# Performance work log

Measured on AMD Instinct MI355X. Metric: run time of the kernel, lower is better.

The kernel has to match this reference:

```python
import jax, jax.numpy as jnp
import numpy as np

D_MODEL, HEADS, D_FF = 1024, 16, 4096
D_K = D_MODEL // HEADS
EPS = 1e-5


def layer_norm(x, g, b):
    mu = jnp.mean(x, axis=-1, keepdims=True)
    var = jnp.mean((x - mu) ** 2, axis=-1, keepdims=True)
    return (x - mu) * jax.lax.rsqrt(var + EPS) * g + b


def setup_inputs() -> dict:
    key = jax.random.key(0)
    ks = jax.random.split(key, 16)
    B, S = 2, 2048
    s = 0.02
    return {
        "src": jax.random.normal(ks[0], (B, S, D_MODEL), jnp.float32),
        "corr": jax.random.normal(ks[1], (B, S, S), jnp.float32),
        "pos": jax.random.normal(ks[2], (B, S, D_MODEL), jnp.float32),
        "Wq": jax.random.normal(ks[3], (D_MODEL, D_MODEL), jnp.float32) * s,
        "bq": jnp.zeros((D_MODEL,), jnp.float32),
        "Wk": jax.random.normal(ks[4], (D_MODEL, D_MODEL), jnp.float32) * s,
        "bk": jnp.zeros((D_MODEL,), jnp.float32),
        "Wv": jax.random.normal(ks[5], (D_MODEL, D_MODEL), jnp.float32) * s,
        "bv": jnp.zeros((D_MODEL,), jnp.float32),
        "Wo": jax.random.normal(ks[6], (D_MODEL, D_MODEL), jnp.float32) * s,
        "bo": jnp.zeros((D_MODEL,), jnp.float32),
        "W1": jax.random.normal(ks[7], (D_MODEL, D_FF), jnp.float32) * s,
        "b1": jnp.zeros((D_FF,), jnp.float32),
        "W2": jax.random.normal(ks[8], (D_FF, D_MODEL), jnp.float32) * s,
        "b2": jnp.zeros((D_MODEL,), jnp.float32),
        "g1": jnp.ones((D_MODEL,), jnp.float32),
        "be1": jnp.zeros((D_MODEL,), jnp.float32),
        "g2": jnp.ones((D_MODEL,), jnp.float32),
        "be2": jnp.zeros((D_MODEL,), jnp.float32),
    }


def reference(src, corr, pos, Wq, bq, Wk, bk, Wv, bv, Wo, bo, W1, b1, W2, b2, g1, be1, g2, be2):
    B, S, _ = src.shape
    qk_in = src + pos  # with_pos_embed for q and k; value uses raw src
    # QKV projections -> [B, H, S, d_k]
    def split_heads(x):
        return x.reshape(B, S, HEADS, D_K).transpose(0, 2, 1, 3)
    q = split_heads(qk_in @ Wq + bq)
    k = split_heads(qk_in @ Wk + bk)
    v = split_heads(src @ Wv + bv)
    # scores [B, H, S, S] with additive correlation bias before softmax
    scores = jnp.einsum("bhqd,bhkd->bhqk", q, k) / jnp.sqrt(jnp.float32(D_K))
    scores = scores + corr[:, None, :, :]
    attn = jax.nn.softmax(scores, axis=-1)
    ctx = jnp.einsum("bhqk,bhkd->bhqd", attn, v)
    concat = ctx.transpose(0, 2, 1, 3).reshape(B, S, D_MODEL)
    attn_out = concat @ Wo + bo
    # post-norm residual blocks (dropout = identity in eval)
    x = layer_norm(src + attn_out, g1, be1)
    ffn = jax.nn.relu(x @ W1 + b1) @ W2 + b2
    x = layer_norm(x + ffn, g2, be2)
    return x
```

## Files before the change

### kernel.cpp

```cpp
#include <hip/hip_runtime.h>
#include <hip/hip_bf16.h>

#define S_LEN  2048
#define BATCH  2
#define DMODEL 1024
#define NHEAD  16
#define DHEAD  64
#define DFF    4096
#define NTOK   (BATCH * S_LEN)
#define QKVLD  3072

typedef __attribute__((ext_vector_type(8))) short short8;
typedef __attribute__((ext_vector_type(4))) short short4v;
typedef __attribute__((ext_vector_type(4))) float f32x4;

__device__ __forceinline__ short f2bs(float f) {
  __hip_bfloat16 h = __float2bfloat16(f);
  short s;
  __builtin_memcpy(&s, &h, sizeof(short));
  return s;
}

__device__ __forceinline__ f32x4 mfma16(short8 a, short8 b, f32x4 c) {
  return __builtin_amdgcn_mfma_f32_16x16x32_bf16(a, b, c, 0, 0, 0);
}

__device__ __forceinline__ void load_lds16(const short* g, short* l) {
  __builtin_amdgcn_global_load_lds(
      (const __attribute__((address_space(1))) void*)g,
      (__attribute__((address_space(3))) void*)l, 16, 0, 0);
}

__global__ void transpose_cast(const float* __restrict__ in, short* __restrict__ out,
                               int R, int C, float scale) {
  __shared__ float tile[32][33];
  const int c0 = blockIdx.x * 32, r0 = blockIdx.y * 32;
  const int tx = threadIdx.x, ty = threadIdx.y;
#pragma unroll
  for (int i = 0; i < 32; i += 8)
    tile[ty + i][tx] = in[(size_t)(r0 + ty + i) * C + c0 + tx];
  __syncthreads();
#pragma unroll
  for (int i = 0; i < 32; i += 8)
    out[(size_t)(c0 + ty + i) * R + r0 + tx] = f2bs(tile[tx][ty + i] * scale);
}

__global__ __launch_bounds__(256) void transpose_bf16(
    const short* __restrict__ in, short* __restrict__ out, int R, int LDin) {
  __shared__ __attribute__((aligned(16))) short tile[64][72];
  const int c0 = blockIdx.x * 64, r0 = blockIdx.y * 64;
#pragma unroll
  for (int i = 0; i < 2; i++) {
    const int idx = threadIdx.x + 256 * i;
    const int rr = idx >> 3, cc8 = (idx & 7) * 8;
    *(int4*)(&tile[rr][cc8]) = *(const int4*)(in + (size_t)(r0 + rr) * LDin + c0 + cc8);
  }
  __syncthreads();
#pragma unroll
  for (int i = 0; i < 2; i++) {
    const int idx = threadIdx.x + 256 * i;
    const int rr = idx >> 3, cc8 = (idx & 7) * 8;
    short8 v;
#pragma unroll
    for (int j = 0; j < 8; j++) v[j] = tile[cc8 + j][rr];
    *(short8*)(out + (size_t)(c0 + rr) * R + r0 + cc8) = v;
  }
}

__global__ void concat_bias(const float* __restrict__ bq, const float* __restrict__ bk,
                            const float* __restrict__ bv, float* __restrict__ bqkv) {
  const int i = blockIdx.x * 256 + threadIdx.x;
  float v;
  if (i < DMODEL) v = bq[i] * 0.125f;
  else if (i < 2 * DMODEL) v = bk[i - DMODEL];
  else v = bv[i - 2 * DMODEL];
  bqkv[i] = v;
}

__global__ void prep_tokens(const float* __restrict__ src, const float* __restrict__ pos,
                            short* __restrict__ qkb, short* __restrict__ srcb) {
  const int i = (blockIdx.x * blockDim.x + threadIdx.x) * 4;
  float4 s = *(const float4*)(src + i);
  float4 p = *(const float4*)(pos + i);
  short4v q4 = {f2bs(s.x + p.x), f2bs(s.y + p.y), f2bs(s.z + p.z), f2bs(s.w + p.w)};
  short4v s4 = {f2bs(s.x), f2bs(s.y), f2bs(s.z), f2bs(s.w)};
  *(short4v*)(qkb + i) = q4;
  *(short4v*)(srcb + i) = s4;
}

template <int RELU, int OUT_BF16>
__global__ __launch_bounds__(256) void gemm_bt(
    const short* __restrict__ A0, const short* __restrict__ A1,
    const short* __restrict__ Bt, const float* __restrict__ bias,
    float* __restrict__ Cf, short* __restrict__ Cb,
    int M, int N, int K, int splitcol) {
  __shared__ __attribute__((aligned(16))) short As[128 * 32];
  __shared__ __attribute__((aligned(16))) short Bs[128 * 32];

  const int tid = threadIdx.x;
  const int wave = tid >> 6, lane = tid & 63;
  const int lm = lane & 15, lq = lane >> 4;
  const int row0 = blockIdx.y * 128, col0 = blockIdx.x * 128;
  const int wr = (wave >> 1) * 64, wc = (wave & 1) * 64;

  const short* A = (col0 < splitcol) ? A0 : A1;
  const short* ag = A + (size_t)(row0 + wave * 32 + (lane >> 2)) * K + (lane & 3) * 8;
  const short* bg = Bt + (size_t)(col0 + wave * 32 + (lane >> 2)) * K + (lane & 3) * 8;
  short* asl = &As[wave * 32 * 32];
  short* bsl = &Bs[wave * 32 * 32];

  f32x4 acc[4][4];
#pragma unroll
  for (int i = 0; i < 4; i++)
#pragma unroll
    for (int j = 0; j < 4; j++) acc[i][j] = (f32x4){0.f, 0.f, 0.f, 0.f};

  for (int k0 = 0; k0 < K; k0 += 32) {
    load_lds16(ag + k0, asl);
    load_lds16(ag + (size_t)16 * K + k0, asl + 16 * 32);
    load_lds16(bg + k0, bsl);
    load_lds16(bg + (size_t)16 * K + k0, bsl + 16 * 32);
    __syncthreads();

    short8 af[4], bfr[4];
#pragma unroll
    for (int i = 0; i < 4; i++)
      af[i] = *(const short8*)(&As[(wr + 16 * i + lm) * 32 + lq * 8]);
#pragma unroll
    for (int j = 0; j < 4; j++)
      bfr[j] = *(const short8*)(&Bs[(wc + 16 * j + lm) * 32 + lq * 8]);
#pragma unroll
    for (int i = 0; i < 4; i++)
#pragma unroll
      for (int j = 0; j < 4; j++) acc[i][j] = mfma16(af[i], bfr[j], acc[i][j]);
    __syncthreads();
  }

#pragma unroll
  for (int i = 0; i < 4; i++) {
#pragma unroll
    for (int j = 0; j < 4; j++) {
      const int col = col0 + wc + 16 * j + lm;
      const float bs = bias[col];
#pragma unroll
      for (int r = 0; r < 4; r++) {
        const int row = row0 + wr + 16 * i + lq * 4 + r;
        float v = acc[i][j][r] + bs;
        if (RELU) v = fmaxf(v, 0.f);
        if (OUT_BF16)
          Cb[(size_t)row * N + col] = f2bs(v);
        else
          Cf[(size_t)row * N + col] = v;
      }
    }
  }
}

template <int RELU, int OUT_BF16>
__global__ __launch_bounds__(256) void gemm_bt64(
    const short* __restrict__ A, const short* __restrict__ Bt,
    const float* __restrict__ bias, float* __restrict__ Cf, short* __restrict__ Cb,
    int M, int N, int K) {
  __shared__ __attribute__((aligned(16))) short As[128 * 32];
  __shared__ __attribute__((aligned(16))) short Bs[64 * 32];

  const int tid = threadIdx.x;
  const int wave = tid >> 6, lane = tid & 63;
  const int lm = lane & 15, lq = lane >> 4;
  const int row0 = blockIdx.y * 128, col0 = blockIdx.x * 64;
  const int wr = (wave >> 1) * 64, wc = (wave & 1) * 32;

  const short* ag = A + (size_t)(row0 + wave * 32 + (lane >> 2)) * K + (lane & 3) * 8;
  const short* bg = Bt + (size_t)(col0 + wave * 16 + (lane >> 2)) * K + (lane & 3) * 8;
  short* asl = &As[wave * 32 * 32];
  short* bsl = &Bs[wave * 16 * 32];

  f32x4 acc[4][2];
#pragma unroll
  for (int i = 0; i < 4; i++)
#pragma unroll
    for (int j = 0; j < 2; j++) acc[i][j] = (f32x4){0.f, 0.f, 0.f, 0.f};

  for (int k0 = 0; k0 < K; k0 += 32) {
    load_lds16(ag + k0, asl);
    load_lds16(ag + (size_t)16 * K + k0, asl + 16 * 32);
    load_lds16(bg + k0, bsl);
    __syncthreads();

    short8 af[4], bfr[2];
#pragma unroll
    for (int i = 0; i < 4; i++)
      af[i] = *(const short8*)(&As[(wr + 16 * i + lm) * 32 + lq * 8]);
#pragma unroll
    for (int j = 0; j < 2; j++)
      bfr[j] = *(const short8*)(&Bs[(wc + 16 * j + lm) * 32 + lq * 8]);
#pragma unroll
    for (int i = 0; i < 4; i++)
#pragma unroll
      for (int j = 0; j < 2; j++) acc[i][j] = mfma16(af[i], bfr[j], acc[i][j]);
    __syncthreads();
  }

#pragma unroll
  for (int i = 0; i < 4; i++) {
#pragma unroll
    for (int j = 0; j < 2; j++) {
      const int col = col0 + wc + 16 * j + lm;
      const float bs = bias[col];
#pragma unroll
      for (int r = 0; r < 4; r++) {
        const int row = row0 + wr + 16 * i + lq * 4 + r;
        float v = acc[i][j][r] + bs;
        if (RELU) v = fmaxf(v, 0.f);
        if (OUT_BF16)
          Cb[(size_t)row * N + col] = f2bs(v);
        else
          Cf[(size_t)row * N + col] = v;
      }
    }
  }
}

__global__ __launch_bounds__(256) void attn_kernel(
    const short* __restrict__ QKV,
    const short* __restrict__ VT,
    const float* __restrict__ corr,
    float* __restrict__ Op,
    float* __restrict__ lp) {
  const int h = blockIdx.x, qtile = blockIdx.y;
  const int b = blockIdx.z >> 1, split = blockIdx.z & 1;
  const int koff = split * (S_LEN / 2);
  const int tid = threadIdx.x;
  const int wave = tid >> 6, lane = tid & 63;
  const int lm = lane & 15, lq = lane >> 4;
  const int qb = qtile * 128 + wave * 32;

  __shared__ __attribute__((aligned(16))) short Ks[64][72];
  __shared__ __attribute__((aligned(16))) short Vs[64][72];
  __shared__ __attribute__((aligned(16))) short Ps[4][32][72];

  const short* q0 = QKV + (size_t)(b * S_LEN + qb + lm) * QKVLD + h * DHEAD;
  const short* q1 = q0 + (size_t)16 * QKVLD;
  const short8 qA0 = *(const short8*)(q0 + lq * 8);
  const short8 qA1 = *(const short8*)(q0 + lq * 8 + 32);
  const short8 qB0 = *(const short8*)(q1 + lq * 8);
  const short8 qB1 = *(const short8*)(q1 + lq * 8 + 32);

  f32x4 oA[4], oB[4];
#pragma unroll
  for (int t = 0; t < 4; t++) {
    oA[t] = (f32x4){0.f, 0.f, 0.f, 0.f};
    oB[t] = (f32x4){0.f, 0.f, 0.f, 0.f};
  }
  f32x4 laccA = (f32x4){0.f, 0.f, 0.f, 0.f};
  f32x4 laccB = (f32x4){0.f, 0.f, 0.f, 0.f};

  const short* Kp = QKV + (size_t)(b * S_LEN) * QKVLD + h * DHEAD + DMODEL;
  const short* Vp = VT + (size_t)(h * DHEAD) * NTOK + b * S_LEN;
  const float* cp0 = corr + (size_t)(b * S_LEN + qb + lm) * S_LEN;
  const float* cp1 = cp0 + (size_t)16 * S_LEN;

  const int srow = tid >> 2;
  const int sc8 = (tid & 3) * 8;

  for (int kt = koff; kt < koff + S_LEN / 2; kt += 64) {
    const short* kr = Kp + (size_t)(kt + srow) * QKVLD + sc8;
    const short* vr = Vp + (size_t)srow * NTOK + kt + sc8;
    *(int4*)(&Ks[srow][sc8]) = *(const int4*)kr;
    *(int4*)(&Ks[srow][sc8 + 32]) = *(const int4*)(kr + 32);
    *(int4*)(&Vs[srow][sc8]) = *(const int4*)vr;
    *(int4*)(&Vs[srow][sc8 + 32]) = *(const int4*)(vr + 32);
    __syncthreads();

    f32x4 svA[4], svB[4];
#pragma unroll
    for (int t = 0; t < 4; t++) {
      const short8 kf0 = *(const short8*)(&Ks[t * 16 + lm][lq * 8]);
      const short8 kf1 = *(const short8*)(&Ks[t * 16 + lm][32 + lq * 8]);
      f32x4 a = (f32x4){0.f, 0.f, 0.f, 0.f};
      a = mfma16(kf0, qA0, a);
      a = mfma16(kf1, qA1, a);
      svA[t] = a;
      f32x4 c = (f32x4){0.f, 0.f, 0.f, 0.f};
      c = mfma16(kf0, qB0, c);
      c = mfma16(kf1, qB1, c);
      svB[t] = c;
    }

#pragma unroll
    for (int t = 0; t < 4; t++) {
      const f32x4 cA = *(const f32x4*)(cp0 + kt + t * 16 + lq * 4);
      const f32x4 cB = *(const f32x4*)(cp1 + kt + t * 16 + lq * 4);
      svA[t] += cA;
      svB[t] += cB;
#pragma unroll
      for (int r = 0; r < 4; r++) {
        svA[t][r] = __expf(svA[t][r]);
        svB[t][r] = __expf(svB[t][r]);
      }
      laccA += svA[t];
      laccB += svB[t];
      short4v pA = {f2bs(svA[t][0]), f2bs(svA[t][1]), f2bs(svA[t][2]), f2bs(svA[t][3])};
      short4v pB = {f2bs(svB[t][0]), f2bs(svB[t][1]), f2bs(svB[t][2]), f2bs(svB[t][3])};
      *(short4v*)(&Ps[wave][lm][t * 16 + lq * 4]) = pA;
      *(short4v*)(&Ps[wave][16 + lm][t * 16 + lq * 4]) = pB;
    }

    const short8 pA0 = *(const short8*)(&Ps[wave][lm][lq * 8]);
    const short8 pA1 = *(const short8*)(&Ps[wave][lm][32 + lq * 8]);
    const short8 pB0 = *(const short8*)(&Ps[wave][16 + lm][lq * 8]);
    const short8 pB1 = *(const short8*)(&Ps[wave][16 + lm][32 + lq * 8]);
#pragma unroll
    for (int t = 0; t < 4; t++) {
      const short8 vf0 = *(const short8*)(&Vs[t * 16 + lm][lq * 8]);
      const short8 vf1 = *(const short8*)(&Vs[t * 16 + lm][32 + lq * 8]);
      oA[t] = mfma16(vf0, pA0, oA[t]);
      oA[t] = mfma16(vf1, pA1, oA[t]);
      oB[t] = mfma16(vf0, pB0, oB[t]);
      oB[t] = mfma16(vf1, pB1, oB[t]);
    }
    __syncthreads();
  }

  float lA = laccA[0] + laccA[1] + laccA[2] + laccA[3];
  float lB = laccB[0] + laccB[1] + laccB[2] + laccB[3];
  lA += __shfl_xor(lA, 16);
  lA += __shfl_xor(lA, 32);
  lB += __shfl_xor(lB, 16);
  lB += __shfl_xor(lB, 32);
  if (lq == 0) {
    lp[((size_t)split * NTOK + b * S_LEN + qb + lm) * NHEAD + h] = lA;
    lp[((size_t)split * NTOK + b * S_LEN + qb + 16 + lm) * NHEAD + h] = lB;
  }
  float* opA = Op + (size_t)split * NTOK * DMODEL +
               (size_t)(b * S_LEN + qb + lm) * DMODEL + h * DHEAD;
  float* opB = opA + (size_t)16 * DMODEL;
#pragma unroll
  for (int t = 0; t < 4; t++) {
    *(f32x4*)(opA + t * 16 + lq * 4) = oA[t];
    *(f32x4*)(opB + t * 16 + lq * 4) = oB[t];
  }
}

__global__ __launch_bounds__(256) void combine_ctx(
    const float* __restrict__ Op, const float* __restrict__ lp,
    short* __restrict__ ctx) {
  const size_t idx = ((size_t)blockIdx.x * 256 + threadIdx.x) * 4;
  const int token = (int)(idx >> 10);
  const int d = (int)(idx & 1023);
  const int h = d >> 6;
  const f32x4 o0 = *(const f32x4*)(Op + idx);
  const f32x4 o1 = *(const f32x4*)(Op + (size_t)NTOK * DMODEL + idx);
  const float l0 = lp[(size_t)token * NHEAD + h];
  const float l1 = lp[((size_t)NTOK + token) * NHEAD + h];
  const float inv = 1.0f / (l0 + l1);
  short4v ov = {f2bs((o0[0] + o1[0]) * inv), f2bs((o0[1] + o1[1]) * inv),
                f2bs((o0[2] + o1[2]) * inv), f2bs((o0[3] + o1[3]) * inv)};
  *(short4v*)(ctx + idx) = ov;
}

__global__ __launch_bounds__(256) void residual_ln(
    const float* __restrict__ xa, const float* __restrict__ xb,
    const float* __restrict__ g, const float* __restrict__ be,
    float* __restrict__ outf, short* __restrict__ outb) {
  const int row = blockIdx.x;
  const int t = threadIdx.x;
  const size_t base = (size_t)row * DMODEL + t * 4;
  float4 a = *(const float4*)(xa + base);
  float4 b = *(const float4*)(xb + base);
  const float v0 = a.x + b.x, v1 = a.y + b.y, v2 = a.z + b.z, v3 = a.w + b.w;
  float sum = v0 + v1 + v2 + v3;
  float sq = v0 * v0 + v1 * v1 + v2 * v2 + v3 * v3;
#pragma unroll
  for (int off = 1; off < 64; off <<= 1) {
    sum += __shfl_xor(sum, off);
    sq += __shfl_xor(sq, off);
  }
  __shared__ float ssum[4], ssq[4];
  const int wave = t >> 6;
  if ((t & 63) == 0) { ssum[wave] = sum; ssq[wave] = sq; }
  __syncthreads();
  sum = ssum[0] + ssum[1] + ssum[2] + ssum[3];
  sq = ssq[0] + ssq[1] + ssq[2] + ssq[3];
  const float mean = sum * (1.0f / DMODEL);
  const float var = sq * (1.0f / DMODEL) - mean * mean;
  const float rstd = rsqrtf(var + 1e-5f);
  float4 gv = *(const float4*)(g + t * 4);
  float4 bv = *(const float4*)(be + t * 4);
  const float o0 = (v0 - mean) * rstd * gv.x + bv.x;
  const float o1 = (v1 - mean) * rstd * gv.y + bv.y;
  const float o2 = (v2 - mean) * rstd * gv.z + bv.z;
  const float o3 = (v3 - mean) * rstd * gv.w + bv.w;
  if (outf) {
    float4 ov = {o0, o1, o2, o3};
    *(float4*)(outf + base) = ov;
  }
  if (outb) {
    short4v ob = {f2bs(o0), f2bs(o1), f2bs(o2), f2bs(o3)};
    *(short4v*)(outb + base) = ob;
  }
}

extern "C" void kernel_launch(void* const* d_in, const int* in_sizes, int n_in,
                              void* d_out, int out_size, void* d_ws, size_t ws_size,
                              hipStream_t stream) {
  const float* src = (const float*)d_in[0];
  const float* corr = (const float*)d_in[1];
  const float* pos = (const float*)d_in[2];
  const float* Wq = (const float*)d_in[3];
  const float* bq = (const float*)d_in[4];
  const float* Wk = (const float*)d_in[5];
  const float* bk = (const float*)d_in[6];
  const float* Wv = (const float*)d_in[7];
  const float* bv = (const float*)d_in[8];
  const float* Wo = (const float*)d_in[9];
  const float* bo = (const float*)d_in[10];
  const float* W1 = (const float*)d_in[11];
  const float* b1 = (const float*)d_in[12];
  const float* W2 = (const float*)d_in[13];
  const float* b2 = (const float*)d_in[14];
  const float* g1 = (const float*)d_in[15];
  const float* be1 = (const float*)d_in[16];
  const float* g2 = (const float*)d_in[17];
  const float* be2 = (const float*)d_in[18];
  float* out = (float*)d_out;

  char* ws = (char*)d_ws;
  size_t off = 0;
  auto alloc = [&](size_t bytes) {
    char* p = ws + off;
    off += (bytes + 255) & ~(size_t)255;
    return p;
  };
  short* WqkvT = (short*)alloc((size_t)QKVLD * DMODEL * 2);
  short* WoT = (short*)alloc((size_t)DMODEL * DMODEL * 2);
  short* W1T = (short*)alloc((size_t)DFF * DMODEL * 2);
  short* W2T = (short*)alloc((size_t)DMODEL * DFF * 2);
  float* bqkv = (float*)alloc((size_t)QKVLD * 4);
  short* qkb = (short*)alloc((size_t)NTOK * DMODEL * 2);
  short* srcb = (short*)alloc((size_t)NTOK * DMODEL * 2);
  short* QKVb = (short*)alloc((size_t)NTOK * QKVLD * 2);
  short* VTt = (short*)alloc((size_t)DMODEL * NTOK * 2);
  short* ctxb = (short*)alloc((size_t)NTOK * DMODEL * 2);
  float* lp = (float*)alloc((size_t)2 * NTOK * NHEAD * 4);
  float* attn_out = (float*)alloc((size_t)NTOK * DMODEL * 4);
  float* x1f = (float*)alloc((size_t)NTOK * DMODEL * 4);
  short* x1b = (short*)alloc((size_t)NTOK * DMODEL * 2);
  short* Hb = (short*)alloc((size_t)NTOK * DFF * 2);
  float* Op = (float*)Hb;
  float* Yf = attn_out;

  const dim3 tb(32, 8);
  transpose_cast<<<dim3(32, 32), tb, 0, stream>>>(Wq, WqkvT, DMODEL, DMODEL, 0.125f);
  transpose_cast<<<dim3(32, 32), tb, 0, stream>>>(Wk, WqkvT + (size_t)DMODEL * DMODEL,
                                                  DMODEL, DMODEL, 1.0f);
  transpose_cast<<<dim3(32, 32), tb, 0, stream>>>(Wv, WqkvT + (size_t)2 * DMODEL * DMODEL,
                                                  DMODEL, DMODEL, 1.0f);
  transpose_cast<<<dim3(32, 32), tb, 0, stream>>>(Wo, WoT, DMODEL, DMODEL, 1.0f);
  transpose_cast<<<dim3(128, 32), tb, 0, stream>>>(W1, W1T, DMODEL, DFF, 1.0f);
  transpose_cast<<<dim3(32, 128), tb, 0, stream>>>(W2, W2T, DFF, DMODEL, 1.0f);
  concat_bias<<<QKVLD / 256, 256, 0, stream>>>(bq, bk, bv, bqkv);

  prep_tokens<<<(NTOK * DMODEL) / (256 * 4), 256, 0, stream>>>(src, pos, qkb, srcb);

  gemm_bt<0, 1><<<dim3(QKVLD / 128, NTOK / 128), 256, 0, stream>>>(
      qkb, srcb, WqkvT, bqkv, nullptr, QKVb, NTOK, QKVLD, DMODEL, 2048);

  transpose_bf16<<<dim3(DMODEL / 64, NTOK / 64), 256, 0, stream>>>(
      QKVb + 2048, VTt, NTOK, QKVLD);

  attn_kernel<<<dim3(NHEAD, S_LEN / 128, BATCH * 2), 256, 0, stream>>>(
      QKVb, VTt, corr, Op, lp);
  combine_ctx<<<(NTOK * DMODEL) / (256 * 4), 256, 0, stream>>>(Op, lp, ctxb);

  gemm_bt64<0, 0><<<dim3(DMODEL / 64, NTOK / 128), 256, 0, stream>>>(
      ctxb, WoT, bo, attn_out, nullptr, NTOK, DMODEL, DMODEL);

  residual_ln<<<NTOK, 256, 0, stream>>>(src, attn_out, g1, be1, x1f, x1b);

  gemm_bt<1, 1><<<dim3(DFF / 128, NTOK / 128), 256, 0, stream>>>(
      x1b, x1b, W1T, b1, nullptr, Hb, NTOK, DFF, DMODEL, 1 << 30);
  gemm_bt64<0, 0><<<dim3(DMODEL / 64, NTOK / 128), 256, 0, stream>>>(
      Hb, W2T, b2, Yf, nullptr, NTOK, DMODEL, DFF);

  residual_ln<<<NTOK, 256, 0, stream>>>(x1f, Yf, g2, be2, out, nullptr);
}
```

Baseline: 527.4 us.

## Use bf16 corr bias, LDS-free attention loads, and split-K atomic GEMMs

Adds a pre-pass that converts the fp32 correlation bias to bf16 so the attention kernel reads half the bytes. The attention kernel now loads K and V fragments straight from global memory instead of staging them through shared memory, which removes two block barriers per tile, and it gets a launch-bounds occupancy hint. The Wo and W2 GEMMs switch from 128x64 tiles to 128x128 split-K tiles that accumulate into a bias-initialised fp32 buffer with atomic adds. In exchange the code adds an extra full pass over corr plus bias-init kernels, atomic traffic, and more uncoalesced global loads in attention.

Measured after the change: 634.9 us. 1.2x slower.

```diff
diff --git a/kernel.cpp b/kernel.cpp
--- a/kernel.cpp
+++ b/kernel.cpp
@@ -19,6 +19,13 @@
   short s;
   __builtin_memcpy(&s, &h, sizeof(short));
   return s;
+}
+
+__device__ __forceinline__ float bs2f(short s) {
+  unsigned u = ((unsigned)(unsigned short)s) << 16;
+  float f;
+  __builtin_memcpy(&f, &u, sizeof(float));
+  return f;
 }
 
 __device__ __forceinline__ f32x4 mfma16(short8 a, short8 b, f32x4 c) {
@@ -88,6 +95,18 @@
   *(short4v*)(srcb + i) = s4;
 }
 
+__global__ void prep_corr(const float* __restrict__ corr, short* __restrict__ corrb) {
+  const size_t i = ((size_t)blockIdx.x * 256 + threadIdx.x) * 4;
+  float4 c = *(const float4*)(corr + i);
+  short4v o = {f2bs(c.x), f2bs(c.y), f2bs(c.z), f2bs(c.w)};
+  *(short4v*)(corrb + i) = o;
+}
+
+__global__ void init_bias(const float* __restrict__ bias, float* __restrict__ out) {
+  const size_t i = ((size_t)blockIdx.x * 256 + threadIdx.x) * 4;
+  *(f32x4*)(out + i) = *(const f32x4*)(bias + (i & (DMODEL - 1)));
+}
+
 template <int RELU, int OUT_BF16>
 __global__ __launch_bounds__(256) void gemm_bt(
     const short* __restrict__ A0, const short* __restrict__ A1,
@@ -156,75 +175,69 @@
   }
 }
 
-template <int RELU, int OUT_BF16>
-__global__ __launch_bounds__(256) void gemm_bt64(
+__global__ __launch_bounds__(256) void gemm_bt_splitk(
     const short* __restrict__ A, const short* __restrict__ Bt,
-    const float* __restrict__ bias, float* __restrict__ Cf, short* __restrict__ Cb,
-    int M, int N, int K) {
+    float* __restrict__ Cf, int M, int N, int K, int Kslice) {
   __shared__ __attribute__((aligned(16))) short As[128 * 32];
-  __shared__ __attribute__((aligned(16))) short Bs[64 * 32];
+  __shared__ __attribute__((aligned(16))) short Bs[128 * 32];
 
   const int tid = threadIdx.x;
   const int wave = tid >> 6, lane = tid & 63;
   const int lm = lane & 15, lq = lane >> 4;
-  const int row0 = blockIdx.y * 128, col0 = blockIdx.x * 64;
-  const int wr = (wave >> 1) * 64, wc = (wave & 1) * 32;
+  const int row0 = blockIdx.y * 128, col0 = blockIdx.x * 128;
+  const int kbase = blockIdx.z * Kslice;
+  const int wr = (wave >> 1) * 64, wc = (wave & 1) * 64;
 
   const short* ag = A + (size_t)(row0 + wave * 32 + (lane >> 2)) * K + (lane & 3) * 8;
-  const short* bg = Bt + (size_t)(col0 + wave * 16 + (lane >> 2)) * K + (lane & 3) * 8;
+  const short* bg = Bt + (size_t)(col0 + wave * 32 + (lane >> 2)) * K + (lane & 3) * 8;
   short* asl = &As[wave * 32 * 32];
-  short* bsl = &Bs[wave * 16 * 32];
-
-  f32x4 acc[4][2];
+  short* bsl = &Bs[wave * 32 * 32];
+
+  f32x4 acc[4][4];
 #pragma unroll
   for (int i = 0; i < 4; i++)
 #pragma unroll
-    for (int j = 0; j < 2; j++) acc[i][j] = (f32x4){0.f, 0.f, 0.f, 0.f};
-
-  for (int k0 = 0; k0 < K; k0 += 32) {
+    for (int j = 0; j < 4; j++) acc[i][j] = (f32x4){0.f, 0.f, 0.f, 0.f};
+
+  for (int k0 = kbase; k0 < kbase + Kslice; k0 += 32) {
     load_lds16(ag + k0, asl);
     load_lds16(ag + (size_t)16 * K + k0, asl + 16 * 32);
     load_lds16(bg + k0, bsl);
+    load_lds16(bg + (size_t)16 * K + k0, bsl + 16 * 32);
     __syncthreads();
 
-    short8 af[4], bfr[2];
+    short8 af[4], bfr[4];
 #pragma unroll
     for (int i = 0; i < 4; i++)
       af[i] = *(const short8*)(&As[(wr + 16 * i + lm) * 32 + lq * 8]);
 #pragma unroll
-    for (int j = 0; j < 2; j++)
+    for (int j = 0; j < 4; j++)
       bfr[j] = *(const short8*)(&Bs[(wc + 16 * j + lm) * 32 + lq * 8]);
 #pragma unroll
     for (int i = 0; i < 4; i++)
 #pragma unroll
-      for (int j = 0; j < 2; j++) acc[i][j] = mfma16(af[i], bfr[j], acc[i][j]);
+      for (int j = 0; j < 4; j++) acc[i][j] = mfma16(af[i], bfr[j], acc[i][j]);
     __syncthreads();
   }
 
 #pragma unroll
   for (int i = 0; i < 4; i++) {
 #pragma unroll
-    for (int j = 0; j < 2; j++) {
+    for (int j = 0; j < 4; j++) {
       const int col = col0 + wc + 16 * j + lm;
-      const float bs = bias[col];
 #pragma unroll
       for (int r = 0; r < 4; r++) {
         const int row = row0 + wr + 16 * i + lq * 4 + r;
-        float v = acc[i][j][r] + bs;
-        if (RELU) v = fmaxf(v, 0.f);
-        if (OUT_BF16)
-          Cb[(size_t)row * N + col] = f2bs(v);
-        else
-          Cf[(size_t)row * N + col] = v;
+        unsafeAtomicAdd(&Cf[(size_t)row * N + col], acc[i][j][r]);
       }
     }
   }
 }
 
-__global__ __launch_bounds__(256) void attn_kernel(
+__global__ __launch_bounds__(256, 4) void attn_kernel(
     const short* __restrict__ QKV,
     const short* __restrict__ VT,
-    const float* __restrict__ corr,
+    const short* __restrict__ corrb,
     float* __restrict__ Op,
     float* __restrict__ lp) {
   const int h = blockIdx.x, qtile = blockIdx.y;
@@ -235,8 +248,6 @@
   const int lm = lane & 15, lq = lane >> 4;
   const int qb = qtile * 128 + wave * 32;
 
-  __shared__ __attribute__((aligned(16))) short Ks[64][72];
-  __shared__ __attribute__((aligned(16))) short Vs[64][72];
   __shared__ __attribute__((aligned(16))) short Ps[4][32][72];
 
   const short* q0 = QKV + (size_t)(b * S_LEN + qb + lm) * QKVLD + h * DHEAD;
@@ -255,28 +266,25 @@
   f32x4 laccA = (f32x4){0.f, 0.f, 0.f, 0.f};
   f32x4 laccB = (f32x4){0.f, 0.f, 0.f, 0.f};
 
-  const short* Kp = QKV + (size_t)(b * S_LEN) * QKVLD + h * DHEAD + DMODEL;
-  const short* Vp = VT + (size_t)(h * DHEAD) * NTOK + b * S_LEN;
-  const float* cp0 = corr + (size_t)(b * S_LEN + qb + lm) * S_LEN;
-  const float* cp1 = cp0 + (size_t)16 * S_LEN;
-
-  const int srow = tid >> 2;
-  const int sc8 = (tid & 3) * 8;
+  const short* Kbase = QKV + (size_t)(b * S_LEN) * QKVLD + DMODEL + h * DHEAD + lq * 8;
+  const short* Vbase = VT + (size_t)(h * DHEAD + lm) * NTOK + b * S_LEN + lq * 8;
+  const short* c0 = corrb + (size_t)(b * S_LEN + qb + lm) * S_LEN;
+  const short* c1 = c0 + (size_t)16 * S_LEN;
 
   for (int kt = koff; kt < koff + S_LEN / 2; kt += 64) {
-    const short* kr = Kp + (size_t)(kt + srow) * QKVLD + sc8;
-    const short* vr = Vp + (size_t)srow * NTOK + kt + sc8;
-    *(int4*)(&Ks[srow][sc8]) = *(const int4*)kr;
-    *(int4*)(&Ks[srow][sc8 + 32]) = *(const int4*)(kr + 32);
-    *(int4*)(&Vs[srow][sc8]) = *(const int4*)vr;
-    *(int4*)(&Vs[srow][sc8 + 32]) = *(const int4*)(vr + 32);
-    __syncthreads();
+    short4v crA[4], crB[4];
+#pragma unroll
+    for (int t = 0; t < 4; t++) {
+      crA[t] = *(const short4v*)(c0 + kt + t * 16 + lq * 4);
+      crB[t] = *(const short4v*)(c1 + kt + t * 16 + lq * 4);
+    }
 
     f32x4 svA[4], svB[4];
 #pragma unroll
     for (int t = 0; t < 4; t++) {
-      const short8 kf0 = *(const short8*)(&Ks[t * 16 + lm][lq * 8]);
-      const short8 kf1 = *(const short8*)(&Ks[t * 16 + lm][32 + lq * 8]);
+      const short* kp = Kbase + (size_t)(kt + t * 16 + lm) * QKVLD;
+      const short8 kf0 = *(const short8*)kp;
+      const short8 kf1 = *(const short8*)(kp + 32);
       f32x4 a = (f32x4){0.f, 0.f, 0.f, 0.f};
       a = mfma16(kf0, qA0, a);
       a = mfma16(kf1, qA1, a);
@@ -289,14 +297,10 @@
 
 #pragma unroll
     for (int t = 0; t < 4; t++) {
-      const f32x4 cA = *(const f32x4*)(cp0 + kt + t * 16 + lq * 4);
-      const f32x4 cB = *(const f32x4*)(cp1 + kt + t * 16 + lq * 4);
-      svA[t] += cA;
-      svB[t] += cB;
 #pragma unroll
       for (int r = 0; r < 4; r++) {
-        svA[t][r] = __expf(svA[t][r]);
-        svB[t][r] = __expf(svB[t][r]);
+        svA[t][r] = __expf(svA[t][r] + bs2f(crA[t][r]));
+        svB[t][r] = __expf(svB[t][r] + bs2f(crB[t][r]));
       }
       laccA += svA[t];
       laccB += svB[t];
@@ -312,14 +316,14 @@
     const short8 pB1 = *(const short8*)(&Ps[wave][16 + lm][32 + lq * 8]);
 #pragma unroll
     for (int t = 0; t < 4; t++) {
-      const short8 vf0 = *(const short8*)(&Vs[t * 16 + lm][lq * 8]);
-      const short8 vf1 = *(const short8*)(&Vs[t * 16 + lm][32 + lq * 8]);
+      const short* vp = Vbase + (size_t)(t * 16) * NTOK + kt;
+      const short8 vf0 = *(const short8*)vp;
+      const short8 vf1 = *(const short8*)(vp + 32);
       oA[t] = mfma16(vf0, pA0, oA[t]);
       oA[t] = mfma16(vf1, pA1, oA[t]);
       oB[t] = mfma16(vf0, pB0, oB[t]);
       oB[t] = mfma16(vf1, pB1, oB[t]);
     }
-    __syncthreads();
   }
 
   float lA = laccA[0] + laccA[1] + laccA[2] + laccA[3];
@@ -441,6 +445,7 @@
   short* srcb = (short*)alloc((size_t)NTOK * DMODEL * 2);
   short* QKVb = (short*)alloc((size_t)NTOK * QKVLD * 2);
   short* VTt = (short*)alloc((size_t)DMODEL * NTOK * 2);
+  short* corrb = (short*)alloc((size_t)BATCH * S_LEN * S_LEN * 2);
   short* ctxb = (short*)alloc((size_t)NTOK * DMODEL * 2);
   float* lp = (float*)alloc((size_t)2 * NTOK * NHEAD * 4);
   float* attn_out = (float*)alloc((size_t)NTOK * DMODEL * 4);
@@ -462,6 +467,7 @@
   concat_bias<<<QKVLD / 256, 256, 0, stream>>>(bq, bk, bv, bqkv);
 
   prep_tokens<<<(NTOK * DMODEL) / (256 * 4), 256, 0, stream>>>(src, pos, qkb, srcb);
+  prep_corr<<<(BATCH * S_LEN * S_LEN) / (256 * 4), 256, 0, stream>>>(corr, corrb);
 
   gemm_bt<0, 1><<<dim3(QKVLD / 128, NTOK / 128), 256, 0, stream>>>(
       qkb, srcb, WqkvT, bqkv, nullptr, QKVb, NTOK, QKVLD, DMODEL, 2048);
@@ -470,18 +476,21 @@
       QKVb + 2048, VTt, NTOK, QKVLD);
 
   attn_kernel<<<dim3(NHEAD, S_LEN / 128, BATCH * 2), 256, 0, stream>>>(
-      QKVb, VTt, corr, Op, lp);
+      QKVb, VTt, corrb, Op, lp);
   combine_ctx<<<(NTOK * DMODEL) / (256 * 4), 256, 0, stream>>>(Op, lp, ctxb);
 
-  gemm_bt64<0, 0><<<dim3(DMODEL / 64, NTOK / 128), 256, 0, stream>>>(
-      ctxb, WoT, bo, attn_out, nullptr, NTOK, DMODEL, DMODEL);
+  init_bias<<<(NTOK * DMODEL) / (256 * 4), 256, 0, stream>>>(bo, attn_out);
+  gemm_bt_splitk<<<dim3(DMODEL / 128, NTOK / 128, 2), 256, 0, stream>>>(
+      ctxb, WoT, attn_out, NTOK, DMODEL, DMODEL, DMODEL / 2);
 
   residual_ln<<<NTOK, 256, 0, stream>>>(src, attn_out, g1, be1, x1f, x1b);
 
   gemm_bt<1, 1><<<dim3(DFF / 128, NTOK / 128), 256, 0, stream>>>(
       x1b, x1b, W1T, b1, nullptr, Hb, NTOK, DFF, DMODEL, 1 << 30);
-  gemm_bt64<0, 0><<<dim3(DMODEL / 64, NTOK / 128), 256, 0, stream>>>(
-      Hb, W2T, b2, Yf, nullptr, NTOK, DMODEL, DFF);
+
+  init_bias<<<(NTOK * DMODEL) / (256 * 4), 256, 0, stream>>>(b2, Yf);
+  gemm_bt_splitk<<<dim3(DMODEL / 128, NTOK / 128, 4), 256, 0, stream>>>(
+      Hb, W2T, Yf, NTOK, DMODEL, DFF, DFF / 4);
 
   residual_ln<<<NTOK, 256, 0, stream>>>(x1f, Yf, g2, be2, out, nullptr);
 }
```
